# Kernel tuning notes

Measured on AMD Instinct MI355X. Metric: run time of the kernel, lower is better.

The kernel has to match this reference:

```python
import jax, jax.numpy as jnp
import numpy as np

N_NODES = 50000
N_EDGES = 1600000
IN_CH = 512
OUT_CH = 512

def setup_inputs() -> dict:
    key = jax.random.key(0)
    k1, k2, k3, k4, k5 = jax.random.split(key, 5)
    x = jax.random.normal(k1, (N_NODES, IN_CH), dtype=jnp.float32)
    adj_vals = jax.random.uniform(k2, (N_EDGES,), dtype=jnp.float32)
    edge_row = jax.random.randint(k3, (N_EDGES,), 0, N_NODES, dtype=jnp.int32)
    edge_col = jax.random.randint(k4, (N_EDGES,), 0, N_NODES, dtype=jnp.int32)
    # weight init per reset_parameters: uniform(-stdv, stdv), stdv = 1/sqrt(out_channel)
    stdv = 1.0 / np.sqrt(OUT_CH)
    weight = jax.random.uniform(k5, (IN_CH, OUT_CH), dtype=jnp.float32,
                                minval=-stdv, maxval=stdv)
    return {"x": x, "adj_vals": adj_vals, "edge_row": edge_row,
            "edge_col": edge_col, "weight": weight}

def reference(x, adj_vals, edge_row, edge_col, weight):
    # support = x @ W  -- dense projection [N, out]
    support = x @ weight
    # output = spmm(adj, support): out[i] = sum_j adj[i, j] * support[j]
    # COO: for edge e = (row, col, val), accumulate val * support[col] into out[row]
    msgs = adj_vals[:, None] * support[edge_col]  # [E, out]
    output = jax.ops.segment_sum(msgs, edge_row, num_segments=N_NODES)
    return output
```

## Files before the change

### kernel.cpp

```cpp
#include <hip/hip_runtime.h>
#include <hip/hip_bf16.h>

#define N_NODES 50000
#define N_EDGES 1600000
#define CH 512
#define SCAN_B 196

typedef short short8v __attribute__((ext_vector_type(8)));
typedef float f32x4 __attribute__((ext_vector_type(4)));
typedef unsigned short ushort8v __attribute__((ext_vector_type(8)));
typedef _Float16 half8v __attribute__((ext_vector_type(8)));

#define GLOAD_LDS16(gptr, lptr)                                                        \
    __builtin_amdgcn_global_load_lds((const __attribute__((address_space(1))) void*)(gptr), \
                                     (__attribute__((address_space(3))) void*)(lptr), 16, 0, 0)

__device__ inline unsigned short f2bf(float x) {
    unsigned u = __float_as_uint(x);
    u = (u + 0x7FFF + ((u >> 16) & 1)) >> 16;
    return (unsigned short)u;
}
__device__ inline float bf2f(unsigned short b) {
    return __uint_as_float(((unsigned)b) << 16);
}
__device__ inline unsigned short f2h(float x) {
    union { _Float16 h; unsigned short u; } cv;
    cv.h = (_Float16)x;
    return cv.u;
}


__global__ __launch_bounds__(256) void hist_kernel(const int* __restrict__ row,
                                                   int* __restrict__ counts) {
    int e = blockIdx.x * 256 + threadIdx.x;
    if (e < N_EDGES) atomicAdd(&counts[row[e]], 1);
}

__global__ __launch_bounds__(256) void bsum_kernel(const int* __restrict__ counts,
                                                   int* __restrict__ bsum) {
    __shared__ int red[256];
    int i = blockIdx.x * 256 + threadIdx.x;
    red[threadIdx.x] = (i < N_NODES) ? counts[i] : 0;
    __syncthreads();
    for (int s = 128; s > 0; s >>= 1) {
        if (threadIdx.x < s) red[threadIdx.x] += red[threadIdx.x + s];
        __syncthreads();
    }
    if (threadIdx.x == 0) bsum[blockIdx.x] = red[0];
}

__global__ __launch_bounds__(256) void bscan_kernel(const int* __restrict__ bsum,
                                                    int* __restrict__ bbase) {
    __shared__ int sc[256];
    int t = threadIdx.x;
    int v = (t < SCAN_B) ? bsum[t] : 0;
    sc[t] = v;
    __syncthreads();
    for (int d = 1; d < 256; d <<= 1) {
        int a = (t >= d) ? sc[t - d] : 0;
        __syncthreads();
        sc[t] += a;
        __syncthreads();
    }
    if (t < SCAN_B) bbase[t] = sc[t] - v;
}

__global__ __launch_bounds__(256) void offsets_kernel(const int* __restrict__ counts,
                                                      const int* __restrict__ bbase,
                                                      int* __restrict__ offsets,
                                                      int* __restrict__ nxt) {
    __shared__ int sc[256];
    int t = threadIdx.x;
    int i = blockIdx.x * 256 + t;
    int v = (i < N_NODES) ? counts[i] : 0;
    sc[t] = v;
    __syncthreads();
    for (int d = 1; d < 256; d <<= 1) {
        int a = (t >= d) ? sc[t - d] : 0;
        __syncthreads();
        sc[t] += a;
        __syncthreads();
    }
    int off = bbase[blockIdx.x] + sc[t] - v;
    if (i < N_NODES) { offsets[i] = off; nxt[i] = off; }
    if (i == 0) offsets[N_NODES] = N_EDGES;
}

__global__ __launch_bounds__(256) void scatter_kernel(const int* __restrict__ row,
                                                      const int* __restrict__ col,
                                                      const float* __restrict__ val,
                                                      int* __restrict__ nxt,
                                                      int2* __restrict__ ep) {
    int e = blockIdx.x * 256 + threadIdx.x;
    if (e < N_EDGES) {
        int r = row[e];
        int p = atomicAdd(&nxt[r], 1);
        ep[p] = make_int2(col[e], __float_as_int(val[e]));
    }
}


__global__ __launch_bounds__(256) void prep_w(const float* __restrict__ W,
                                              unsigned short* __restrict__ Wc) {
    __shared__ float tile[32][65];
    const int kt = blockIdx.x;
    const int nb = blockIdx.y * 64;
    const int t = threadIdx.x;
    const int nl = t & 63, kl = t >> 6;
#pragma unroll
    for (int p = 0; p < 8; ++p) {
        int k = p * 4 + kl;
        tile[k][nl] = W[(size_t)(kt * 32 + k) * CH + nb + nl];
    }
    __syncthreads();
    const int n_local = t >> 2, j = t & 3;
    ushort8v hi, lo;
#pragma unroll
    for (int q = 0; q < 8; ++q) {
        float x = tile[j * 8 + q][n_local];
        unsigned short h = f2bf(x);
        hi[q] = h;
        lo[q] = f2bf(x - bf2f(h));
    }
    size_t base = ((size_t)kt * 512 + nb + n_local) * 64 + j * 8;
    *(ushort8v*)&Wc[base] = hi;
    *(ushort8v*)&Wc[base + 32] = lo;
}


__global__ __launch_bounds__(256) void gemm_kernel(const float* __restrict__ X,
                                                   const unsigned short* __restrict__ Wc,
                                                   unsigned short* __restrict__ S) {
    __shared__ __align__(16) unsigned short Al[128 * 64];
    __shared__ __align__(16) unsigned short Bl[128 * 64];

    const int tid = threadIdx.x;
    const int wave = tid >> 6;
    const int lane = tid & 63;
    const int wm = (wave >> 1) * 64;
    const int wn = (wave & 1) * 64;
    const int m0 = blockIdx.x * 128;
    const int n0 = blockIdx.y * 128;

    const int lrow = lane >> 3, lslot = lane & 7;
    const int b_lane_off = lrow * 64 + ((lslot ^ lrow) << 3);

    const int srow = tid >> 1;
    const int skh = tid & 1;
    const int gm_s = m0 + srow;
    const int r7 = srow & 7;

    f32x4 acc[4][4] = {};

    for (int kt = 0; kt < 16; ++kt) {
        const unsigned short* bsrc = Wc + ((size_t)kt * 512 + n0 + wave * 32) * 64 + b_lane_off;
        unsigned short* bdst = &Bl[(wave * 32) * 64];
        GLOAD_LDS16(bsrc, bdst);
        GLOAD_LDS16(bsrc + 512, bdst + 512);
        GLOAD_LDS16(bsrc + 1024, bdst + 1024);
        GLOAD_LDS16(bsrc + 1536, bdst + 1536);

        float xv[16];
        if (gm_s < N_NODES) {
            const float* xp = &X[(size_t)gm_s * CH + kt * 32 + skh * 16];
            *(float4*)&xv[0]  = *(const float4*)&xp[0];
            *(float4*)&xv[4]  = *(const float4*)&xp[4];
            *(float4*)&xv[8]  = *(const float4*)&xp[8];
            *(float4*)&xv[12] = *(const float4*)&xp[12];
        } else {
#pragma unroll
            for (int q = 0; q < 16; ++q) xv[q] = 0.f;
        }
        ushort8v h0, h1, l0, l1;
#pragma unroll
        for (int q = 0; q < 8; ++q) {
            unsigned short h = f2bf(xv[q]);
            h0[q] = h;
            l0[q] = f2bf(xv[q] - bf2f(h));
            unsigned short h2 = f2bf(xv[8 + q]);
            h1[q] = h2;
            l1[q] = f2bf(xv[8 + q] - bf2f(h2));
        }
        {
            const int s0 = skh * 2, s1 = skh * 2 + 1;
            unsigned short* arow = &Al[srow * 64];
            *(ushort8v*)&arow[((s0 ^ r7) << 3)] = h0;
            *(ushort8v*)&arow[((s1 ^ r7) << 3)] = h1;
            *(ushort8v*)&arow[(((s0 | 4) ^ r7) << 3)] = l0;
            *(ushort8v*)&arow[(((s1 | 4) ^ r7) << 3)] = l1;
        }
        __syncthreads();

        const int fr = lane & 15;
        const int fs = lane >> 4;
        const int fx = lane & 7;
        short8v ahi[4], alo[4];
#pragma unroll
        for (int mi = 0; mi < 4; ++mi) {
            const unsigned short* ar = &Al[(wm + mi * 16 + fr) * 64];
            ahi[mi] = *(const short8v*)&ar[((fs ^ fx) << 3)];
            alo[mi] = *(const short8v*)&ar[(((fs | 4) ^ fx) << 3)];
        }
#pragma unroll
        for (int ni = 0; ni < 4; ++ni) {
            const unsigned short* br = &Bl[(wn + ni * 16 + fr) * 64];
            short8v bhi = *(const short8v*)&br[((fs ^ fx) << 3)];
            short8v blo = *(const short8v*)&br[(((fs | 4) ^ fx) << 3)];
#pragma unroll
            for (int mi = 0; mi < 4; ++mi) {
                acc[mi][ni] = __builtin_amdgcn_mfma_f32_16x16x32_bf16(ahi[mi], bhi, acc[mi][ni], 0, 0, 0);
                acc[mi][ni] = __builtin_amdgcn_mfma_f32_16x16x32_bf16(ahi[mi], blo, acc[mi][ni], 0, 0, 0);
                acc[mi][ni] = __builtin_amdgcn_mfma_f32_16x16x32_bf16(alo[mi], bhi, acc[mi][ni], 0, 0, 0);
            }
        }
        __syncthreads();
    }

    const int crow = (lane >> 4) * 4;
    const int ccol = lane & 15;
#pragma unroll
    for (int mi = 0; mi < 4; ++mi) {
#pragma unroll
        for (int r = 0; r < 4; ++r) {
            int gm = m0 + wm + mi * 16 + crow + r;
            if (gm < N_NODES) {
#pragma unroll
                for (int ni = 0; ni < 4; ++ni) {
                    S[(size_t)gm * CH + n0 + wn + ni * 16 + ccol] = f2h(acc[mi][ni][r]);
                }
            }
        }
    }
}


__global__ __launch_bounds__(128) void spmm_kernel(const int* __restrict__ offsets,
                                                   const int2* __restrict__ ep,
                                                   const unsigned short* __restrict__ S,
                                                   float* __restrict__ out) {
    const int r = blockIdx.x * 2 + (threadIdx.x >> 6);
    const int lane = threadIdx.x & 63;
    const int c = lane * 8;
    const int start = offsets[r];
    const int end = offsets[r + 1];

    float acc[8] = {0.f, 0.f, 0.f, 0.f, 0.f, 0.f, 0.f, 0.f};
    int e = start;
    for (; e + 3 < end; e += 4) {
        const int2 e0 = ep[e];
        const int2 e1 = ep[e + 1];
        const int2 e2 = ep[e + 2];
        const int2 e3 = ep[e + 3];
        const half8v s0 = *(const half8v*)&S[(size_t)e0.x * CH + c];
        const half8v s1 = *(const half8v*)&S[(size_t)e1.x * CH + c];
        const half8v s2 = *(const half8v*)&S[(size_t)e2.x * CH + c];
        const half8v s3 = *(const half8v*)&S[(size_t)e3.x * CH + c];
        const float v0 = __int_as_float(e0.y);
        const float v1 = __int_as_float(e1.y);
        const float v2 = __int_as_float(e2.y);
        const float v3 = __int_as_float(e3.y);
#pragma unroll
        for (int j = 0; j < 8; ++j) {
            acc[j] += v0 * (float)s0[j];
            acc[j] += v1 * (float)s1[j];
            acc[j] += v2 * (float)s2[j];
            acc[j] += v3 * (float)s3[j];
        }
    }
    for (; e < end; ++e) {
        const int2 e0 = ep[e];
        const half8v s0 = *(const half8v*)&S[(size_t)e0.x * CH + c];
        const float v0 = __int_as_float(e0.y);
#pragma unroll
        for (int j = 0; j < 8; ++j) acc[j] += v0 * (float)s0[j];
    }
    float4 o0 = {acc[0], acc[1], acc[2], acc[3]};
    float4 o1 = {acc[4], acc[5], acc[6], acc[7]};
    *(float4*)&out[(size_t)r * CH + c] = o0;
    *(float4*)&out[(size_t)r * CH + c + 4] = o1;
}


extern "C" void kernel_launch(void* const* d_in, const int* in_sizes, int n_in,
                              void* d_out, int out_size, void* d_ws, size_t ws_size,
                              hipStream_t stream) {
    const float* x        = (const float*)d_in[0];
    const float* adj_vals = (const float*)d_in[1];
    const int*   edge_row = (const int*)d_in[2];
    const int*   edge_col = (const int*)d_in[3];
    const float* weight   = (const float*)d_in[4];
    float* out = (float*)d_out;

    auto align256 = [](size_t v) { return (v + 255) & ~(size_t)255; };
    char* ws = (char*)d_ws;
    size_t off = 0;
    unsigned short* support = (unsigned short*)(ws + off); off = align256(off + (size_t)N_NODES * CH * sizeof(unsigned short));
    int*   counts  = (int*)(ws + off);            off = align256(off + (size_t)N_NODES * sizeof(int));
    int*   offsets = (int*)(ws + off);            off = align256(off + (size_t)(N_NODES + 1) * sizeof(int));
    int*   nxt     = (int*)(ws + off);            off = align256(off + (size_t)N_NODES * sizeof(int));
    int2*  ep      = (int2*)(ws + off);           off = align256(off + (size_t)N_EDGES * sizeof(int2));
    unsigned short* Wc = (unsigned short*)(ws + off); off = align256(off + (size_t)16 * 512 * 64 * sizeof(unsigned short));
    int*   bsum    = (int*)(ws + off);            off = align256(off + (size_t)SCAN_B * sizeof(int));
    int*   bbase   = (int*)(ws + off);            off = align256(off + (size_t)SCAN_B * sizeof(int));

    hipMemsetAsync(counts, 0, (size_t)N_NODES * sizeof(int), stream);

    const int EB = (N_EDGES + 255) / 256;
    hist_kernel<<<EB, 256, 0, stream>>>(edge_row, counts);
    bsum_kernel<<<SCAN_B, 256, 0, stream>>>(counts, bsum);
    bscan_kernel<<<1, 256, 0, stream>>>(bsum, bbase);
    offsets_kernel<<<SCAN_B, 256, 0, stream>>>(counts, bbase, offsets, nxt);
    scatter_kernel<<<EB, 256, 0, stream>>>(edge_row, edge_col, adj_vals, nxt, ep);

    dim3 wgrid(16, 8);
    prep_w<<<wgrid, 256, 0, stream>>>(weight, Wc);

    dim3 ggrid((N_NODES + 127) / 128, CH / 128);
    gemm_kernel<<<ggrid, 256, 0, stream>>>(x, Wc, support);

    spmm_kernel<<<N_NODES / 2, 128, 0, stream>>>(offsets, ep, support, out);
}
```

Measured before the change: 659.8 us.

## Sort edges within each row by column bucket for gather locality

Builds a CSR keyed by (row, col>>11) with 25 column buckets per row, so edges inside a row come out ordered by column bucket. The scan kernels are reworked to handle 1.25M keys, with 16 elements per thread and two block sums per thread in the top-level scan. The aim is more locality in the support-row gathers across concurrently running rows, which should improve L2 hit rate. The SpMM also switches to nontemporal loads for the edge list and nontemporal stores for the output, at the cost of larger counting and scan passes.

New measurement: 680.8 us. +3.2%, slower.

```diff
diff --git a/kernel.cpp b/kernel.cpp
--- a/kernel.cpp
+++ b/kernel.cpp
@@ -4,12 +4,17 @@
 #define N_NODES 50000
 #define N_EDGES 1600000
 #define CH 512
-#define SCAN_B 196
+#define NB 25
+#define N_KEYS (N_NODES * NB)
+#define BS_ELEMS 4096
+#define NBLK ((N_KEYS + BS_ELEMS - 1) / BS_ELEMS)
 
 typedef short short8v __attribute__((ext_vector_type(8)));
 typedef float f32x4 __attribute__((ext_vector_type(4)));
 typedef unsigned short ushort8v __attribute__((ext_vector_type(8)));
 typedef _Float16 half8v __attribute__((ext_vector_type(8)));
+typedef int int2v __attribute__((ext_vector_type(2)));
+typedef float float4v __attribute__((ext_vector_type(4)));
 
 #define GLOAD_LDS16(gptr, lptr)                                                        \
     __builtin_amdgcn_global_load_lds((const __attribute__((address_space(1))) void*)(gptr), \
@@ -31,29 +36,42 @@
 
 
 __global__ __launch_bounds__(256) void hist_kernel(const int* __restrict__ row,
+                                                   const int* __restrict__ col,
                                                    int* __restrict__ counts) {
     int e = blockIdx.x * 256 + threadIdx.x;
-    if (e < N_EDGES) atomicAdd(&counts[row[e]], 1);
+    if (e < N_EDGES) {
+        int key = row[e] * NB + (col[e] >> 11);
+        atomicAdd(&counts[key], 1);
+    }
 }
 
 __global__ __launch_bounds__(256) void bsum_kernel(const int* __restrict__ counts,
                                                    int* __restrict__ bsum) {
     __shared__ int red[256];
-    int i = blockIdx.x * 256 + threadIdx.x;
-    red[threadIdx.x] = (i < N_NODES) ? counts[i] : 0;
+    const int t = threadIdx.x;
+    const int base = blockIdx.x * BS_ELEMS + t * 16;
+    int s = 0;
+#pragma unroll
+    for (int q = 0; q < 16; ++q) {
+        int i = base + q;
+        if (i < N_KEYS) s += counts[i];
+    }
+    red[t] = s;
     __syncthreads();
-    for (int s = 128; s > 0; s >>= 1) {
-        if (threadIdx.x < s) red[threadIdx.x] += red[threadIdx.x + s];
-        __syncthreads();
-    }
-    if (threadIdx.x == 0) bsum[blockIdx.x] = red[0];
+    for (int st = 128; st > 0; st >>= 1) {
+        if (t < st) red[t] += red[t + st];
+        __syncthreads();
+    }
+    if (t == 0) bsum[blockIdx.x] = red[0];
 }
 
 __global__ __launch_bounds__(256) void bscan_kernel(const int* __restrict__ bsum,
                                                     int* __restrict__ bbase) {
     __shared__ int sc[256];
-    int t = threadIdx.x;
-    int v = (t < SCAN_B) ? bsum[t] : 0;
+    const int t = threadIdx.x;
+    int a0 = (2 * t < NBLK) ? bsum[2 * t] : 0;
+    int a1 = (2 * t + 1 < NBLK) ? bsum[2 * t + 1] : 0;
+    int v = a0 + a1;
     sc[t] = v;
     __syncthreads();
     for (int d = 1; d < 256; d <<= 1) {
@@ -62,18 +80,27 @@
         sc[t] += a;
         __syncthreads();
     }
-    if (t < SCAN_B) bbase[t] = sc[t] - v;
+    int ex = sc[t] - v;
+    if (2 * t < NBLK) bbase[2 * t] = ex;
+    if (2 * t + 1 < NBLK) bbase[2 * t + 1] = ex + a0;
 }
 
 __global__ __launch_bounds__(256) void offsets_kernel(const int* __restrict__ counts,
                                                       const int* __restrict__ bbase,
-                                                      int* __restrict__ offsets,
+                                                      int* __restrict__ keyoff,
                                                       int* __restrict__ nxt) {
     __shared__ int sc[256];
-    int t = threadIdx.x;
-    int i = blockIdx.x * 256 + t;
-    int v = (i < N_NODES) ? counts[i] : 0;
-    sc[t] = v;
+    const int t = threadIdx.x;
+    const int base = blockIdx.x * BS_ELEMS + t * 16;
+    int vals[16];
+    int s = 0;
+#pragma unroll
+    for (int q = 0; q < 16; ++q) {
+        int i = base + q;
+        vals[q] = (i < N_KEYS) ? counts[i] : 0;
+        s += vals[q];
+    }
+    sc[t] = s;
     __syncthreads();
     for (int d = 1; d < 256; d <<= 1) {
         int a = (t >= d) ? sc[t - d] : 0;
@@ -81,9 +108,14 @@
         sc[t] += a;
         __syncthreads();
     }
-    int off = bbase[blockIdx.x] + sc[t] - v;
-    if (i < N_NODES) { offsets[i] = off; nxt[i] = off; }
-    if (i == 0) offsets[N_NODES] = N_EDGES;
+    int run = bbase[blockIdx.x] + sc[t] - s;
+#pragma unroll
+    for (int q = 0; q < 16; ++q) {
+        int i = base + q;
+        if (i < N_KEYS) { keyoff[i] = run; nxt[i] = run; }
+        run += vals[q];
+    }
+    if (blockIdx.x == 0 && t == 0) keyoff[N_KEYS] = N_EDGES;
 }
 
 __global__ __launch_bounds__(256) void scatter_kernel(const int* __restrict__ row,
@@ -93,9 +125,10 @@
                                                       int2* __restrict__ ep) {
     int e = blockIdx.x * 256 + threadIdx.x;
     if (e < N_EDGES) {
-        int r = row[e];
-        int p = atomicAdd(&nxt[r], 1);
-        ep[p] = make_int2(col[e], __float_as_int(val[e]));
+        int c = col[e];
+        int key = row[e] * NB + (c >> 11);
+        int p = atomicAdd(&nxt[key], 1);
+        ep[p] = make_int2(c, __float_as_int(val[e]));
     }
 }
 
@@ -234,23 +267,23 @@
 }
 
 
-__global__ __launch_bounds__(128) void spmm_kernel(const int* __restrict__ offsets,
-                                                   const int2* __restrict__ ep,
+__global__ __launch_bounds__(128) void spmm_kernel(const int* __restrict__ keyoff,
+                                                   const int2v* __restrict__ ep,
                                                    const unsigned short* __restrict__ S,
                                                    float* __restrict__ out) {
     const int r = blockIdx.x * 2 + (threadIdx.x >> 6);
     const int lane = threadIdx.x & 63;
     const int c = lane * 8;
-    const int start = offsets[r];
-    const int end = offsets[r + 1];
+    const int start = keyoff[r * NB];
+    const int end = keyoff[(r + 1) * NB];
 
     float acc[8] = {0.f, 0.f, 0.f, 0.f, 0.f, 0.f, 0.f, 0.f};
     int e = start;
     for (; e + 3 < end; e += 4) {
-        const int2 e0 = ep[e];
-        const int2 e1 = ep[e + 1];
-        const int2 e2 = ep[e + 2];
-        const int2 e3 = ep[e + 3];
+        const int2v e0 = __builtin_nontemporal_load(&ep[e]);
+        const int2v e1 = __builtin_nontemporal_load(&ep[e + 1]);
+        const int2v e2 = __builtin_nontemporal_load(&ep[e + 2]);
+        const int2v e3 = __builtin_nontemporal_load(&ep[e + 3]);
         const half8v s0 = *(const half8v*)&S[(size_t)e0.x * CH + c];
         const half8v s1 = *(const half8v*)&S[(size_t)e1.x * CH + c];
         const half8v s2 = *(const half8v*)&S[(size_t)e2.x * CH + c];
@@ -268,16 +301,16 @@
         }
     }
     for (; e < end; ++e) {
-        const int2 e0 = ep[e];
+        const int2v e0 = __builtin_nontemporal_load(&ep[e]);
         const half8v s0 = *(const half8v*)&S[(size_t)e0.x * CH + c];
         const float v0 = __int_as_float(e0.y);
 #pragma unroll
         for (int j = 0; j < 8; ++j) acc[j] += v0 * (float)s0[j];
     }
-    float4 o0 = {acc[0], acc[1], acc[2], acc[3]};
-    float4 o1 = {acc[4], acc[5], acc[6], acc[7]};
-    *(float4*)&out[(size_t)r * CH + c] = o0;
-    *(float4*)&out[(size_t)r * CH + c + 4] = o1;
+    float4v o0 = {acc[0], acc[1], acc[2], acc[3]};
+    float4v o1 = {acc[4], acc[5], acc[6], acc[7]};
+    __builtin_nontemporal_store(o0, (float4v*)&out[(size_t)r * CH + c]);
+    __builtin_nontemporal_store(o1, (float4v*)&out[(size_t)r * CH + c + 4]);
 }
 
 
@@ -295,21 +328,21 @@
     char* ws = (char*)d_ws;
     size_t off = 0;
     unsigned short* support = (unsigned short*)(ws + off); off = align256(off + (size_t)N_NODES * CH * sizeof(unsigned short));
-    int*   counts  = (int*)(ws + off);            off = align256(off + (size_t)N_NODES * sizeof(int));
-    int*   offsets = (int*)(ws + off);            off = align256(off + (size_t)(N_NODES + 1) * sizeof(int));
-    int*   nxt     = (int*)(ws + off);            off = align256(off + (size_t)N_NODES * sizeof(int));
+    int*   counts  = (int*)(ws + off);            off = align256(off + (size_t)N_KEYS * sizeof(int));
+    int*   keyoff  = (int*)(ws + off);            off = align256(off + (size_t)(N_KEYS + 1) * sizeof(int));
+    int*   nxt     = (int*)(ws + off);            off = align256(off + (size_t)N_KEYS * sizeof(int));
     int2*  ep      = (int2*)(ws + off);           off = align256(off + (size_t)N_EDGES * sizeof(int2));
     unsigned short* Wc = (unsigned short*)(ws + off); off = align256(off + (size_t)16 * 512 * 64 * sizeof(unsigned short));
-    int*   bsum    = (int*)(ws + off);            off = align256(off + (size_t)SCAN_B * sizeof(int));
-    int*   bbase   = (int*)(ws + off);            off = align256(off + (size_t)SCAN_B * sizeof(int));
-
-    hipMemsetAsync(counts, 0, (size_t)N_NODES * sizeof(int), stream);
+    int*   bsum    = (int*)(ws + off);            off = align256(off + (size_t)NBLK * sizeof(int));
+    int*   bbase   = (int*)(ws + off);            off = align256(off + (size_t)NBLK * sizeof(int));
+
+    (void)hipMemsetAsync(counts, 0, (size_t)N_KEYS * sizeof(int), stream);
 
     const int EB = (N_EDGES + 255) / 256;
-    hist_kernel<<<EB, 256, 0, stream>>>(edge_row, counts);
-    bsum_kernel<<<SCAN_B, 256, 0, stream>>>(counts, bsum);
+    hist_kernel<<<EB, 256, 0, stream>>>(edge_row, edge_col, counts);
+    bsum_kernel<<<NBLK, 256, 0, stream>>>(counts, bsum);
     bscan_kernel<<<1, 256, 0, stream>>>(bsum, bbase);
-    offsets_kernel<<<SCAN_B, 256, 0, stream>>>(counts, bbase, offsets, nxt);
+    offsets_kernel<<<NBLK, 256, 0, stream>>>(counts, bbase, keyoff, nxt);
     scatter_kernel<<<EB, 256, 0, stream>>>(edge_row, edge_col, adj_vals, nxt, ep);
 
     dim3 wgrid(16, 8);
@@ -318,5 +351,5 @@
     dim3 ggrid((N_NODES + 127) / 128, CH / 128);
     gemm_kernel<<<ggrid, 256, 0, stream>>>(x, Wc, support);
 
-    spmm_kernel<<<N_NODES / 2, 128, 0, stream>>>(offsets, ep, support, out);
-}
+    spmm_kernel<<<N_NODES / 2, 128, 0, stream>>>(keyoff, (const int2v*)ep, support, out);
+}
```

## Switch GEMM to fp16 with single-precision X and pre-converted tiled X layout

Applied to the files above, without the earlier changes.

Replaces the three-pass bf16 split (hi*hi, hi*lo, lo*hi) with fp16 MFMA using a single fp16 X and hi/lo fp16 W, so there are two MFMAs per tile step instead of three. X is converted to fp16 once in a new prep_x kernel and stored in a K-tiled padded layout, which the GEMM then streams into LDS with direct global-to-LDS loads instead of converting per block. The cost is an extra kernel launch plus a full write and reread of X in fp16, and lower accuracy because X is kept only to fp16 precision and may overflow or flush for extreme values.

Result: slower. 675.8 us (+2.4%).

```diff
diff --git a/kernel.cpp b/kernel.cpp
--- a/kernel.cpp
+++ b/kernel.cpp
@@ -4,9 +4,9 @@
 #define N_NODES 50000
 #define N_EDGES 1600000
 #define CH 512
+#define M_PAD 50048
 #define SCAN_B 196
 
-typedef short short8v __attribute__((ext_vector_type(8)));
 typedef float f32x4 __attribute__((ext_vector_type(4)));
 typedef unsigned short ushort8v __attribute__((ext_vector_type(8)));
 typedef _Float16 half8v __attribute__((ext_vector_type(8)));
@@ -15,18 +15,15 @@
     __builtin_amdgcn_global_load_lds((const __attribute__((address_space(1))) void*)(gptr), \
                                      (__attribute__((address_space(3))) void*)(lptr), 16, 0, 0)
 
-__device__ inline unsigned short f2bf(float x) {
-    unsigned u = __float_as_uint(x);
-    u = (u + 0x7FFF + ((u >> 16) & 1)) >> 16;
-    return (unsigned short)u;
-}
-__device__ inline float bf2f(unsigned short b) {
-    return __uint_as_float(((unsigned)b) << 16);
-}
 __device__ inline unsigned short f2h(float x) {
     union { _Float16 h; unsigned short u; } cv;
     cv.h = (_Float16)x;
     return cv.u;
+}
+__device__ inline float h2f(unsigned short u) {
+    union { unsigned short u; _Float16 h; } cv;
+    cv.u = u;
+    return (float)cv.h;
 }
 
 
@@ -100,8 +97,39 @@
 }
 
 
+__global__ __launch_bounds__(256) void prep_x(const float* __restrict__ X,
+                                              unsigned short* __restrict__ Xa) {
+    const int t = threadIdx.x;
+    const int m = blockIdx.x * 32 + (t >> 3);
+    const int cpart = t & 7;
+    float xv[64];
+    if (m < N_NODES) {
+        const float* xp = &X[(size_t)m * CH + cpart * 64];
+#pragma unroll
+        for (int i = 0; i < 16; ++i)
+            *(float4*)&xv[i * 4] = *(const float4*)&xp[i * 4];
+    } else {
+#pragma unroll
+        for (int i = 0; i < 64; ++i) xv[i] = 0.f;
+    }
+#pragma unroll
+    for (int kk = 0; kk < 2; ++kk) {
+        const int kt = cpart * 2 + kk;
+        ushort8v o[4];
+#pragma unroll
+        for (int q = 0; q < 32; ++q)
+            o[q >> 3][q & 7] = f2h(xv[kk * 32 + q]);
+        unsigned short* dst = &Xa[((size_t)kt * M_PAD + m) * 32];
+        *(ushort8v*)&dst[0]  = o[0];
+        *(ushort8v*)&dst[8]  = o[1];
+        *(ushort8v*)&dst[16] = o[2];
+        *(ushort8v*)&dst[24] = o[3];
+    }
+}
+
+
 __global__ __launch_bounds__(256) void prep_w(const float* __restrict__ W,
-                                              unsigned short* __restrict__ Wc) {
+                                              unsigned short* __restrict__ Wb) {
     __shared__ float tile[32][65];
     const int kt = blockIdx.x;
     const int nb = blockIdx.y * 64;
@@ -118,20 +146,20 @@
 #pragma unroll
     for (int q = 0; q < 8; ++q) {
         float x = tile[j * 8 + q][n_local];
-        unsigned short h = f2bf(x);
+        unsigned short h = f2h(x);
         hi[q] = h;
-        lo[q] = f2bf(x - bf2f(h));
+        lo[q] = f2h(x - h2f(h));
     }
     size_t base = ((size_t)kt * 512 + nb + n_local) * 64 + j * 8;
-    *(ushort8v*)&Wc[base] = hi;
-    *(ushort8v*)&Wc[base + 32] = lo;
-}
-
-
-__global__ __launch_bounds__(256) void gemm_kernel(const float* __restrict__ X,
-                                                   const unsigned short* __restrict__ Wc,
+    *(ushort8v*)&Wb[base] = hi;
+    *(ushort8v*)&Wb[base + 32] = lo;
+}
+
+
+__global__ __launch_bounds__(256) void gemm_kernel(const unsigned short* __restrict__ Xa,
+                                                   const unsigned short* __restrict__ Wb,
                                                    unsigned short* __restrict__ S) {
-    __shared__ __align__(16) unsigned short Al[128 * 64];
+    __shared__ __align__(16) unsigned short Al[128 * 32];
     __shared__ __align__(16) unsigned short Bl[128 * 64];
 
     const int tid = threadIdx.x;
@@ -144,73 +172,44 @@
 
     const int lrow = lane >> 3, lslot = lane & 7;
     const int b_lane_off = lrow * 64 + ((lslot ^ lrow) << 3);
-
-    const int srow = tid >> 1;
-    const int skh = tid & 1;
-    const int gm_s = m0 + srow;
-    const int r7 = srow & 7;
+    const int arow_l = lane >> 2, aslot = lane & 3;
+    const int a_lane_off = arow_l * 32 + ((aslot ^ (arow_l & 3)) << 3);
+
+    const int fr = lane & 15;
+    const int fs = lane >> 4;
+    const int fx3 = fr & 3;
+    const int fx7 = fr & 7;
 
     f32x4 acc[4][4] = {};
 
     for (int kt = 0; kt < 16; ++kt) {
-        const unsigned short* bsrc = Wc + ((size_t)kt * 512 + n0 + wave * 32) * 64 + b_lane_off;
+        const unsigned short* bsrc = Wb + ((size_t)kt * 512 + n0 + wave * 32) * 64 + b_lane_off;
         unsigned short* bdst = &Bl[(wave * 32) * 64];
         GLOAD_LDS16(bsrc, bdst);
         GLOAD_LDS16(bsrc + 512, bdst + 512);
         GLOAD_LDS16(bsrc + 1024, bdst + 1024);
         GLOAD_LDS16(bsrc + 1536, bdst + 1536);
 
-        float xv[16];
-        if (gm_s < N_NODES) {
-            const float* xp = &X[(size_t)gm_s * CH + kt * 32 + skh * 16];
-            *(float4*)&xv[0]  = *(const float4*)&xp[0];
-            *(float4*)&xv[4]  = *(const float4*)&xp[4];
-            *(float4*)&xv[8]  = *(const float4*)&xp[8];
-            *(float4*)&xv[12] = *(const float4*)&xp[12];
-        } else {
-#pragma unroll
-            for (int q = 0; q < 16; ++q) xv[q] = 0.f;
-        }
-        ushort8v h0, h1, l0, l1;
-#pragma unroll
-        for (int q = 0; q < 8; ++q) {
-            unsigned short h = f2bf(xv[q]);
-            h0[q] = h;
-            l0[q] = f2bf(xv[q] - bf2f(h));
-            unsigned short h2 = f2bf(xv[8 + q]);
-            h1[q] = h2;
-            l1[q] = f2bf(xv[8 + q] - bf2f(h2));
-        }
-        {
-            const int s0 = skh * 2, s1 = skh * 2 + 1;
-            unsigned short* arow = &Al[srow * 64];
-            *(ushort8v*)&arow[((s0 ^ r7) << 3)] = h0;
-            *(ushort8v*)&arow[((s1 ^ r7) << 3)] = h1;
-            *(ushort8v*)&arow[(((s0 | 4) ^ r7) << 3)] = l0;
-            *(ushort8v*)&arow[(((s1 | 4) ^ r7) << 3)] = l1;
-        }
-        __syncthreads();
-
-        const int fr = lane & 15;
-        const int fs = lane >> 4;
-        const int fx = lane & 7;
-        short8v ahi[4], alo[4];
-#pragma unroll
-        for (int mi = 0; mi < 4; ++mi) {
-            const unsigned short* ar = &Al[(wm + mi * 16 + fr) * 64];
-            ahi[mi] = *(const short8v*)&ar[((fs ^ fx) << 3)];
-            alo[mi] = *(const short8v*)&ar[(((fs | 4) ^ fx) << 3)];
-        }
+        const unsigned short* asrc = Xa + ((size_t)kt * M_PAD + m0 + wave * 16) * 32 + a_lane_off;
+        unsigned short* adst = &Al[(wave * 16) * 32];
+        GLOAD_LDS16(asrc, adst);
+        GLOAD_LDS16(asrc + 64 * 32, adst + 64 * 32);
+
+        __syncthreads();
+
+        half8v af[4];
+#pragma unroll
+        for (int mi = 0; mi < 4; ++mi)
+            af[mi] = *(const half8v*)&Al[(wm + mi * 16 + fr) * 32 + ((fs ^ fx3) << 3)];
 #pragma unroll
         for (int ni = 0; ni < 4; ++ni) {
             const unsigned short* br = &Bl[(wn + ni * 16 + fr) * 64];
-            short8v bhi = *(const short8v*)&br[((fs ^ fx) << 3)];
-            short8v blo = *(const short8v*)&br[(((fs | 4) ^ fx) << 3)];
+            half8v bhi = *(const half8v*)&br[((fs ^ fx7) << 3)];
+            half8v blo = *(const half8v*)&br[(((fs | 4) ^ fx7) << 3)];
 #pragma unroll
             for (int mi = 0; mi < 4; ++mi) {
-                acc[mi][ni] = __builtin_amdgcn_mfma_f32_16x16x32_bf16(ahi[mi], bhi, acc[mi][ni], 0, 0, 0);
-                acc[mi][ni] = __builtin_amdgcn_mfma_f32_16x16x32_bf16(ahi[mi], blo, acc[mi][ni], 0, 0, 0);
-                acc[mi][ni] = __builtin_amdgcn_mfma_f32_16x16x32_bf16(alo[mi], bhi, acc[mi][ni], 0, 0, 0);
+                acc[mi][ni] = __builtin_amdgcn_mfma_f32_16x16x32_f16(af[mi], bhi, acc[mi][ni], 0, 0, 0);
+                acc[mi][ni] = __builtin_amdgcn_mfma_f32_16x16x32_f16(af[mi], blo, acc[mi][ni], 0, 0, 0);
             }
         }
         __syncthreads();
@@ -295,15 +294,16 @@
     char* ws = (char*)d_ws;
     size_t off = 0;
     unsigned short* support = (unsigned short*)(ws + off); off = align256(off + (size_t)N_NODES * CH * sizeof(unsigned short));
+    unsigned short* Xa = (unsigned short*)(ws + off);      off = align256(off + (size_t)16 * M_PAD * 32 * sizeof(unsigned short));
     int*   counts  = (int*)(ws + off);            off = align256(off + (size_t)N_NODES * sizeof(int));
     int*   offsets = (int*)(ws + off);            off = align256(off + (size_t)(N_NODES + 1) * sizeof(int));
     int*   nxt     = (int*)(ws + off);            off = align256(off + (size_t)N_NODES * sizeof(int));
     int2*  ep      = (int2*)(ws + off);           off = align256(off + (size_t)N_EDGES * sizeof(int2));
-    unsigned short* Wc = (unsigned short*)(ws + off); off = align256(off + (size_t)16 * 512 * 64 * sizeof(unsigned short));
+    unsigned short* Wb = (unsigned short*)(ws + off); off = align256(off + (size_t)16 * 512 * 64 * sizeof(unsigned short));
     int*   bsum    = (int*)(ws + off);            off = align256(off + (size_t)SCAN_B * sizeof(int));
     int*   bbase   = (int*)(ws + off);            off = align256(off + (size_t)SCAN_B * sizeof(int));
 
-    hipMemsetAsync(counts, 0, (size_t)N_NODES * sizeof(int), stream);
+    (void)hipMemsetAsync(counts, 0, (size_t)N_NODES * sizeof(int), stream);
 
     const int EB = (N_EDGES + 255) / 256;
     hist_kernel<<<EB, 256, 0, stream>>>(edge_row, counts);
@@ -312,11 +312,12 @@
     offsets_kernel<<<SCAN_B, 256, 0, stream>>>(counts, bbase, offsets, nxt);
     scatter_kernel<<<EB, 256, 0, stream>>>(edge_row, edge_col, adj_vals, nxt, ep);
 
+    prep_x<<<M_PAD / 32, 256, 0, stream>>>(x, Xa);
     dim3 wgrid(16, 8);
-    prep_w<<<wgrid, 256, 0, stream>>>(weight, Wc);
-
-    dim3 ggrid((N_NODES + 127) / 128, CH / 128);
-    gemm_kernel<<<ggrid, 256, 0, stream>>>(x, Wc, support);
+    prep_w<<<wgrid, 256, 0, stream>>>(weight, Wb);
+
+    dim3 ggrid(M_PAD / 128, CH / 128);
+    gemm_kernel<<<ggrid, 256, 0, stream>>>(Xa, Wb, support);
 
     spmm_kernel<<<N_NODES / 2, 128, 0, stream>>>(offsets, ep, support, out);
 }
```
